# Kernel tuning notes

Measured on AMD Instinct MI355X. Metric: run time of the kernel, lower is better.

Reference implementation:

```python
import jax, jax.numpy as jnp
import numpy as np

SEQ_LEN = 8192
HIDDEN = 2048


def setup_inputs() -> dict:
    key = jax.random.key(0)
    ks = jax.random.split(key, 7)
    scale = 1.0 / np.sqrt(HIDDEN)
    return {
        "hidden": jax.random.normal(ks[0], (1, HIDDEN), dtype=jnp.float32),
        "encoder_outputs": jax.random.normal(ks[1], (SEQ_LEN, HIDDEN), dtype=jnp.float32),
        "pool_output": jax.random.normal(ks[2], (1, HIDDEN), dtype=jnp.float32),
        # nn.Linear(hidden, hidden) params for attn_pool_q and attn_q_hidden
        "W_pq": jax.random.uniform(ks[3], (HIDDEN, HIDDEN), jnp.float32, -scale, scale),
        "b_pq": jax.random.uniform(ks[4], (HIDDEN,), jnp.float32, -scale, scale),
        "W_qh": jax.random.uniform(ks[5], (HIDDEN, HIDDEN), jnp.float32, -scale, scale),
        "b_qh": jax.random.uniform(ks[6], (HIDDEN,), jnp.float32, -scale, scale),
    }


def reference(hidden, encoder_outputs, pool_output, W_pq, b_pq, W_qh, b_qh):
    # Batched form of the original per-step 'general' score loop:
    #   e_i = hidden . ( W_qh @ (enc_i * (W_pq @ pool + b_pq)) + b_qh )
    m = pool_output.reshape(-1) @ W_pq.T + b_pq          # (H,)  attn_pool_q(pool)
    gated = encoder_outputs * m[None, :]                 # (S, H) enc_i * energy
    e = gated @ W_qh.T + b_qh                            # (S, H) attn_q_hidden(.)
    energies = e @ hidden.reshape(-1)                    # (S,)  dot with hidden
    # F.softmax over the seq dim, then .unsqueeze(0).unsqueeze(0) -> (1,1,S)
    return jax.nn.softmax(energies)[None, None, :]
```

## Files before the change

### kernel.cpp

```cpp
#include <hip/hip_runtime.h>
#include <math.h>

#define SEQ 8192
#define HID 2048
#define NC4 (HID / 4)
#define VCHUNKS 8


__global__ __launch_bounds__(256) void k1(const float* __restrict__ pool,
                                          const float* __restrict__ W_pq,
                                          const float* __restrict__ b_pq,
                                          const float* __restrict__ hidden,
                                          const float* __restrict__ W_qh,
                                          float* __restrict__ m,
                                          float* __restrict__ vpart) {
  const int tid  = threadIdx.x;
  const int wave = tid >> 6;
  const int lane = tid & 63;
  const int bid  = blockIdx.x;

  if (bid < 256) {
    const float4* p4 = reinterpret_cast<const float4*>(pool);
    const int row0 = bid * 8 + wave * 2;
    const float4* W0 = reinterpret_cast<const float4*>(W_pq + (size_t)row0 * HID);
    const float4* W1 = reinterpret_cast<const float4*>(W_pq + (size_t)(row0 + 1) * HID);
    float acc0 = 0.f, acc1 = 0.f;
    #pragma unroll
    for (int j = 0; j < 8; ++j) {
      const int i = lane + j * 64;
      float4 p = p4[i];
      float4 w0 = W0[i], w1 = W1[i];
      acc0 += w0.x * p.x + w0.y * p.y + w0.z * p.z + w0.w * p.w;
      acc1 += w1.x * p.x + w1.y * p.y + w1.z * p.z + w1.w * p.w;
    }
    #pragma unroll
    for (int off = 32; off; off >>= 1) {
      acc0 += __shfl_down(acc0, off, 64);
      acc1 += __shfl_down(acc1, off, 64);
    }
    if (lane == 0) {
      m[row0]     = acc0 + b_pq[row0];
      m[row0 + 1] = acc1 + b_pq[row0 + 1];
    }
  } else {
    __shared__ float4 part[256];
    const int u  = bid - 256;
    const int ct = u & 31;
    const int rc = u >> 5;
    const int c4 = ct * 16 + (tid & 15);
    const int r0 = rc * 256 + (tid >> 4) * 16;
    float4 a0 = {0.f, 0.f, 0.f, 0.f};
    float4 a1 = {0.f, 0.f, 0.f, 0.f};
    #pragma unroll
    for (int i = 0; i < 8; ++i) {
      const int ra = r0 + i, rb = r0 + 8 + i;
      const float  ha = hidden[ra],  hb = hidden[rb];
      const float4 wa = reinterpret_cast<const float4*>(W_qh + (size_t)ra * HID)[c4];
      const float4 wb = reinterpret_cast<const float4*>(W_qh + (size_t)rb * HID)[c4];
      a0.x += ha * wa.x; a0.y += ha * wa.y; a0.z += ha * wa.z; a0.w += ha * wa.w;
      a1.x += hb * wb.x; a1.y += hb * wb.y; a1.z += hb * wb.z; a1.w += hb * wb.w;
    }
    a0.x += a1.x; a0.y += a1.y; a0.z += a1.z; a0.w += a1.w;
    part[tid] = a0;
    __syncthreads();
    if (tid < 16) {
      float4 s = part[tid];
      #pragma unroll
      for (int k = 1; k < 16; ++k) {
        float4 p = part[k * 16 + tid];
        s.x += p.x; s.y += p.y; s.z += p.z; s.w += p.w;
      }
      reinterpret_cast<float4*>(vpart)[rc * NC4 + ct * 16 + tid] = s;
    }
  }
}

__global__ __launch_bounds__(256) void k2(const float* __restrict__ enc,
                                          const float* __restrict__ m,
                                          const float* __restrict__ vpart,
                                          float* __restrict__ energ) {
  __shared__ float4 gl[NC4];
  const int tid  = threadIdx.x;
  const int wave = tid >> 6;
  const int lane = tid & 63;
  const int bid  = blockIdx.x;

  const float4* vp = reinterpret_cast<const float4*>(vpart);
  const float4* m4 = reinterpret_cast<const float4*>(m);
  #pragma unroll
  for (int j = 0; j < 2; ++j) {
    const int c = tid + j * 256;
    float4 a = vp[c];
    #pragma unroll
    for (int k = 1; k < VCHUNKS; ++k) {
      float4 p = vp[k * NC4 + c];
      a.x += p.x; a.y += p.y; a.z += p.z; a.w += p.w;
    }
    const float4 mm = m4[c];
    float4 g = {a.x * mm.x, a.y * mm.y, a.z * mm.z, a.w * mm.w};
    gl[c] = g;
  }
  __syncthreads();

  float4 greg[8];
  #pragma unroll
  for (int j = 0; j < 8; ++j) greg[j] = gl[lane + j * 64];

  const int row0 = bid * 8 + wave * 2;
  const float4* E0 = reinterpret_cast<const float4*>(enc + (size_t)row0 * HID);
  const float4* E1 = reinterpret_cast<const float4*>(enc + (size_t)(row0 + 1) * HID);
  float acc0 = 0.f, acc1 = 0.f;
  #pragma unroll
  for (int j = 0; j < 8; ++j) {
    const int i = lane + j * 64;
    float4 e0 = E0[i], e1 = E1[i], g = greg[j];
    acc0 += e0.x * g.x + e0.y * g.y + e0.z * g.z + e0.w * g.w;
    acc1 += e1.x * g.x + e1.y * g.y + e1.z * g.z + e1.w * g.w;
  }
  #pragma unroll
  for (int off = 32; off; off >>= 1) {
    acc0 += __shfl_down(acc0, off, 64);
    acc1 += __shfl_down(acc1, off, 64);
  }
  if (lane == 0) {
    energ[row0]     = acc0;
    energ[row0 + 1] = acc1;
  }
}

__global__ __launch_bounds__(256) void k3(const float* __restrict__ e,
                                          float* __restrict__ out) {
  __shared__ float red[8];
  const int tid  = threadIdx.x;
  const int wave = tid >> 6;
  const int lane = tid & 63;
  const int bid  = blockIdx.x;

  float vals[32];
  float mx = -INFINITY;
  #pragma unroll
  for (int i = 0; i < 32; ++i) {
    vals[i] = e[tid + i * 256];
    mx = fmaxf(mx, vals[i]);
  }
  #pragma unroll
  for (int off = 32; off; off >>= 1) mx = fmaxf(mx, __shfl_down(mx, off, 64));
  if (lane == 0) red[wave] = mx;
  __syncthreads();
  const float bm = fmaxf(fmaxf(red[0], red[1]), fmaxf(red[2], red[3]));

  float s = 0.f;
  #pragma unroll
  for (int i = 0; i < 32; ++i) s += expf(vals[i] - bm);
  #pragma unroll
  for (int off = 32; off; off >>= 1) s += __shfl_down(s, off, 64);
  if (lane == 0) red[4 + wave] = s;
  __syncthreads();
  const float inv = 1.f / (red[4] + red[5] + red[6] + red[7]);

  const int row = bid * 256 + tid;
  out[row] = expf(e[row] - bm) * inv;
}

extern "C" void kernel_launch(void* const* d_in, const int* in_sizes, int n_in,
                              void* d_out, int out_size, void* d_ws, size_t ws_size,
                              hipStream_t stream) {
  const float* hidden = (const float*)d_in[0];
  const float* enc    = (const float*)d_in[1];
  const float* pool   = (const float*)d_in[2];
  const float* W_pq   = (const float*)d_in[3];
  const float* b_pq   = (const float*)d_in[4];
  const float* W_qh   = (const float*)d_in[5];

  float* out   = (float*)d_out;
  float* ws    = (float*)d_ws;
  float* m     = ws;
  float* vpart = ws + HID;
  float* energ = ws + HID + VCHUNKS * HID;

  k1<<<dim3(512), dim3(256), 0, stream>>>(pool, W_pq, b_pq, hidden, W_qh, m, vpart);
  k2<<<dim3(1024), dim3(256), 0, stream>>>(enc, m, vpart, energ);
  k3<<<dim3(32), dim3(256), 0, stream>>>(energ, out);
}
```

Baseline: 26.99 us.

## Fully reduce W_qh^T·hidden in k1, prefetch enc rows, vectorize softmax loads

The W_qh-transpose-times-hidden reduction now assigns each k1 block eight full columns and reduces across all rows in-block with a shared-memory tree. This writes the final vector directly, so k2 no longer sums eight partial chunks. k2 issues all encoder loads for its two rows up front to raise memory-level parallelism, and adds an occupancy hint to its launch bounds. k3 reads energies as float4. The tree reduction adds seven syncthreads per block, and the k1 W_qh reads become narrow 32-byte column strips per row, which may coalesce poorly.

```diff
diff --git a/kernel.cpp b/kernel.cpp
--- a/kernel.cpp
+++ b/kernel.cpp
@@ -4,7 +4,6 @@
 #define SEQ 8192
 #define HID 2048
 #define NC4 (HID / 4)
-#define VCHUNKS 8
 
 
 __global__ __launch_bounds__(256) void k1(const float* __restrict__ pool,
@@ -13,7 +12,7 @@
                                           const float* __restrict__ hidden,
                                           const float* __restrict__ W_qh,
                                           float* __restrict__ m,
-                                          float* __restrict__ vpart) {
+                                          float* __restrict__ v) {
   const int tid  = threadIdx.x;
   const int wave = tid >> 6;
   const int lane = tid & 63;
@@ -43,61 +42,51 @@
       m[row0 + 1] = acc1 + b_pq[row0 + 1];
     }
   } else {
-    __shared__ float4 part[256];
-    const int u  = bid - 256;
-    const int ct = u & 31;
-    const int rc = u >> 5;
-    const int c4 = ct * 16 + (tid & 15);
-    const int r0 = rc * 256 + (tid >> 4) * 16;
-    float4 a0 = {0.f, 0.f, 0.f, 0.f};
-    float4 a1 = {0.f, 0.f, 0.f, 0.f};
+    __shared__ float4 arr[256];
+    const int c8  = bid - 256;
+    const int fq  = tid & 1;
+    const int rph = tid >> 1;
+    const int c4  = c8 * 2 + fq;
+    float4 acc = {0.f, 0.f, 0.f, 0.f};
     #pragma unroll
-    for (int i = 0; i < 8; ++i) {
-      const int ra = r0 + i, rb = r0 + 8 + i;
-      const float  ha = hidden[ra],  hb = hidden[rb];
-      const float4 wa = reinterpret_cast<const float4*>(W_qh + (size_t)ra * HID)[c4];
-      const float4 wb = reinterpret_cast<const float4*>(W_qh + (size_t)rb * HID)[c4];
-      a0.x += ha * wa.x; a0.y += ha * wa.y; a0.z += ha * wa.z; a0.w += ha * wa.w;
-      a1.x += hb * wb.x; a1.y += hb * wb.y; a1.z += hb * wb.z; a1.w += hb * wb.w;
+    for (int i = 0; i < 16; ++i) {
+      const int r = rph + i * 128;
+      const float  h = hidden[r];
+      const float4 w = reinterpret_cast<const float4*>(W_qh + (size_t)r * HID)[c4];
+      acc.x += h * w.x; acc.y += h * w.y; acc.z += h * w.z; acc.w += h * w.w;
     }
-    a0.x += a1.x; a0.y += a1.y; a0.z += a1.z; a0.w += a1.w;
-    part[tid] = a0;
+    arr[tid] = acc;
     __syncthreads();
-    if (tid < 16) {
-      float4 s = part[tid];
-      #pragma unroll
-      for (int k = 1; k < 16; ++k) {
-        float4 p = part[k * 16 + tid];
-        s.x += p.x; s.y += p.y; s.z += p.z; s.w += p.w;
+    #pragma unroll
+    for (int s = 64; s >= 1; s >>= 1) {
+      if (rph < s) {
+        const float4 o = arr[(rph + s) * 2 + fq];
+        acc.x += o.x; acc.y += o.y; acc.z += o.z; acc.w += o.w;
+        arr[tid] = acc;
       }
-      reinterpret_cast<float4*>(vpart)[rc * NC4 + ct * 16 + tid] = s;
+      __syncthreads();
     }
+    if (rph == 0) reinterpret_cast<float4*>(v)[c4] = acc;
   }
 }
 
-__global__ __launch_bounds__(256) void k2(const float* __restrict__ enc,
-                                          const float* __restrict__ m,
-                                          const float* __restrict__ vpart,
-                                          float* __restrict__ energ) {
+__global__ __launch_bounds__(256, 4) void k2(const float* __restrict__ enc,
+                                             const float* __restrict__ m,
+                                             const float* __restrict__ v,
+                                             float* __restrict__ energ) {
   __shared__ float4 gl[NC4];
   const int tid  = threadIdx.x;
   const int wave = tid >> 6;
   const int lane = tid & 63;
   const int bid  = blockIdx.x;
 
-  const float4* vp = reinterpret_cast<const float4*>(vpart);
   const float4* m4 = reinterpret_cast<const float4*>(m);
+  const float4* v4 = reinterpret_cast<const float4*>(v);
   #pragma unroll
   for (int j = 0; j < 2; ++j) {
     const int c = tid + j * 256;
-    float4 a = vp[c];
-    #pragma unroll
-    for (int k = 1; k < VCHUNKS; ++k) {
-      float4 p = vp[k * NC4 + c];
-      a.x += p.x; a.y += p.y; a.z += p.z; a.w += p.w;
-    }
-    const float4 mm = m4[c];
-    float4 g = {a.x * mm.x, a.y * mm.y, a.z * mm.z, a.w * mm.w};
+    const float4 mm = m4[c], vv = v4[c];
+    float4 g = {mm.x * vv.x, mm.y * vv.y, mm.z * vv.z, mm.w * vv.w};
     gl[c] = g;
   }
   __syncthreads();
@@ -109,13 +98,19 @@
   const int row0 = bid * 8 + wave * 2;
   const float4* E0 = reinterpret_cast<const float4*>(enc + (size_t)row0 * HID);
   const float4* E1 = reinterpret_cast<const float4*>(enc + (size_t)(row0 + 1) * HID);
+
+  float4 e0[8], e1[8];
+  #pragma unroll
+  for (int j = 0; j < 8; ++j) e0[j] = E0[lane + j * 64];
+  #pragma unroll
+  for (int j = 0; j < 8; ++j) e1[j] = E1[lane + j * 64];
+
   float acc0 = 0.f, acc1 = 0.f;
   #pragma unroll
   for (int j = 0; j < 8; ++j) {
-    const int i = lane + j * 64;
-    float4 e0 = E0[i], e1 = E1[i], g = greg[j];
-    acc0 += e0.x * g.x + e0.y * g.y + e0.z * g.z + e0.w * g.w;
-    acc1 += e1.x * g.x + e1.y * g.y + e1.z * g.z + e1.w * g.w;
+    const float4 g = greg[j];
+    acc0 += e0[j].x * g.x + e0[j].y * g.y + e0[j].z * g.z + e0[j].w * g.w;
+    acc1 += e1[j].x * g.x + e1[j].y * g.y + e1[j].z * g.z + e1[j].w * g.w;
   }
   #pragma unroll
   for (int off = 32; off; off >>= 1) {
@@ -136,12 +131,13 @@
   const int lane = tid & 63;
   const int bid  = blockIdx.x;
 
-  float vals[32];
+  const float4* e4 = reinterpret_cast<const float4*>(e);
+  float4 vals[8];
   float mx = -INFINITY;
   #pragma unroll
-  for (int i = 0; i < 32; ++i) {
-    vals[i] = e[tid + i * 256];
-    mx = fmaxf(mx, vals[i]);
+  for (int i = 0; i < 8; ++i) {
+    vals[i] = e4[tid + i * 256];
+    mx = fmaxf(mx, fmaxf(fmaxf(vals[i].x, vals[i].y), fmaxf(vals[i].z, vals[i].w)));
   }
   #pragma unroll
   for (int off = 32; off; off >>= 1) mx = fmaxf(mx, __shfl_down(mx, off, 64));
@@ -151,7 +147,10 @@
 
   float s = 0.f;
   #pragma unroll
-  for (int i = 0; i < 32; ++i) s += expf(vals[i] - bm);
+  for (int i = 0; i < 8; ++i) {
+    s += expf(vals[i].x - bm) + expf(vals[i].y - bm) +
+         expf(vals[i].z - bm) + expf(vals[i].w - bm);
+  }
   #pragma unroll
   for (int off = 32; off; off >>= 1) s += __shfl_down(s, off, 64);
   if (lane == 0) red[4 + wave] = s;
@@ -175,10 +174,10 @@
   float* out   = (float*)d_out;
   float* ws    = (float*)d_ws;
   float* m     = ws;
-  float* vpart = ws + HID;
-  float* energ = ws + HID + VCHUNKS * HID;
+  float* v     = ws + HID;
+  float* energ = ws + 2 * HID;
 
-  k1<<<dim3(512), dim3(256), 0, stream>>>(pool, W_pq, b_pq, hidden, W_qh, m, vpart);
-  k2<<<dim3(1024), dim3(256), 0, stream>>>(enc, m, vpart, energ);
+  k1<<<dim3(512), dim3(256), 0, stream>>>(pool, W_pq, b_pq, hidden, W_qh, m, v);
+  k2<<<dim3(1024), dim3(256), 0, stream>>>(enc, m, v, energ);
   k3<<<dim3(32), dim3(256), 0, stream>>>(energ, out);
 }
```

After: 34.18 us. +26.6%, slower.

## Fuse softmax into energy kernel via last-block atomic counter

Applied to the files above, without the earlier changes.

Drops the third kernel launch. k2 now increments a global counter after writing its energies, and the last block to finish computes the full softmax over all 8192 energies in one block. k1 resets the counter each call. This removes one launch and its gap, but the softmax now runs on a single block instead of 32, and every block pays for an acq_rel atomic.

```diff
diff --git a/kernel.cpp b/kernel.cpp
--- a/kernel.cpp
+++ b/kernel.cpp
@@ -5,6 +5,7 @@
 #define HID 2048
 #define NC4 (HID / 4)
 #define VCHUNKS 8
+#define NBK2 1024
 
 
 __global__ __launch_bounds__(256) void k1(const float* __restrict__ pool,
@@ -13,11 +14,14 @@
                                           const float* __restrict__ hidden,
                                           const float* __restrict__ W_qh,
                                           float* __restrict__ m,
-                                          float* __restrict__ vpart) {
+                                          float* __restrict__ vpart,
+                                          unsigned* __restrict__ counter) {
   const int tid  = threadIdx.x;
   const int wave = tid >> 6;
   const int lane = tid & 63;
   const int bid  = blockIdx.x;
+
+  if (bid == 0 && tid == 0) *counter = 0u;
 
   if (bid < 256) {
     const float4* p4 = reinterpret_cast<const float4*>(pool);
@@ -78,8 +82,12 @@
 __global__ __launch_bounds__(256) void k2(const float* __restrict__ enc,
                                           const float* __restrict__ m,
                                           const float* __restrict__ vpart,
-                                          float* __restrict__ energ) {
+                                          float* __restrict__ energ,
+                                          unsigned* __restrict__ counter,
+                                          float* __restrict__ out) {
   __shared__ float4 gl[NC4];
+  __shared__ float red[8];
+  __shared__ unsigned oldv;
   const int tid  = threadIdx.x;
   const int wave = tid >> 6;
   const int lane = tid & 63;
@@ -123,24 +131,22 @@
     acc1 += __shfl_down(acc1, off, 64);
   }
   if (lane == 0) {
-    energ[row0]     = acc0;
-    energ[row0 + 1] = acc1;
+    __hip_atomic_store(&energ[row0],     acc0, __ATOMIC_RELAXED, __HIP_MEMORY_SCOPE_AGENT);
+    __hip_atomic_store(&energ[row0 + 1], acc1, __ATOMIC_RELAXED, __HIP_MEMORY_SCOPE_AGENT);
   }
-}
 
-__global__ __launch_bounds__(256) void k3(const float* __restrict__ e,
-                                          float* __restrict__ out) {
-  __shared__ float red[8];
-  const int tid  = threadIdx.x;
-  const int wave = tid >> 6;
-  const int lane = tid & 63;
-  const int bid  = blockIdx.x;
+  if (tid == 0) {
+    oldv = __hip_atomic_fetch_add(counter, 1u, __ATOMIC_ACQ_REL, __HIP_MEMORY_SCOPE_AGENT);
+  }
+  __syncthreads();
+  if (oldv != NBK2 - 1) return;
 
   float vals[32];
   float mx = -INFINITY;
   #pragma unroll
   for (int i = 0; i < 32; ++i) {
-    vals[i] = e[tid + i * 256];
+    vals[i] = __hip_atomic_load(&energ[tid + i * 256], __ATOMIC_RELAXED,
+                                __HIP_MEMORY_SCOPE_AGENT);
     mx = fmaxf(mx, vals[i]);
   }
   #pragma unroll
@@ -151,15 +157,18 @@
 
   float s = 0.f;
   #pragma unroll
-  for (int i = 0; i < 32; ++i) s += expf(vals[i] - bm);
+  for (int i = 0; i < 32; ++i) {
+    vals[i] = expf(vals[i] - bm);
+    s += vals[i];
+  }
   #pragma unroll
   for (int off = 32; off; off >>= 1) s += __shfl_down(s, off, 64);
   if (lane == 0) red[4 + wave] = s;
   __syncthreads();
   const float inv = 1.f / (red[4] + red[5] + red[6] + red[7]);
 
-  const int row = bid * 256 + tid;
-  out[row] = expf(e[row] - bm) * inv;
+  #pragma unroll
+  for (int i = 0; i < 32; ++i) out[tid + i * 256] = vals[i] * inv;
 }
 
 extern "C" void kernel_launch(void* const* d_in, const int* in_sizes, int n_in,
@@ -172,13 +181,14 @@
   const float* b_pq   = (const float*)d_in[4];
   const float* W_qh   = (const float*)d_in[5];
 
-  float* out   = (float*)d_out;
-  float* ws    = (float*)d_ws;
-  float* m     = ws;
-  float* vpart = ws + HID;
-  float* energ = ws + HID + VCHUNKS * HID;
+  float*    out     = (float*)d_out;
+  float*    ws      = (float*)d_ws;
+  float*    m       = ws;
+  float*    vpart   = ws + HID;
+  float*    energ   = ws + HID + VCHUNKS * HID;
+  unsigned* counter = (unsigned*)(ws + HID + VCHUNKS * HID + SEQ);
 
-  k1<<<dim3(512), dim3(256), 0, stream>>>(pool, W_pq, b_pq, hidden, W_qh, m, vpart);
-  k2<<<dim3(1024), dim3(256), 0, stream>>>(enc, m, vpart, energ);
-  k3<<<dim3(32), dim3(256), 0, stream>>>(energ, out);
+  k1<<<dim3(512), dim3(256), 0, stream>>>(pool, W_pq, b_pq, hidden, W_qh,
+                                          m, vpart, counter);
+  k2<<<dim3(NBK2), dim3(256), 0, stream>>>(enc, m, vpart, energ, counter, out);
 }
```

New measurement: 58.67 us. 2.17x slower.
